# Kernel optimization log

Hardware: AMD Instinct MI355X
Metric: run time of the kernel (lower is better)

The kernel has to match this reference:

```python
import jax, jax.numpy as jnp
import numpy as np

HIDDEN = 2048
NUM_HEADS = 16
HEAD_DIM = HIDDEN // NUM_HEADS
SCALE = 1.0 / np.sqrt(HEAD_DIM).astype(np.float32)
BATCH, SEQ = 2, 2048


def setup_inputs() -> dict:
    key = jax.random.key(0)
    ks = jax.random.split(key, 9)
    std = 0.02
    inp = {
        'hidden_states': jax.random.normal(ks[0], (BATCH, SEQ, HIDDEN), jnp.float32),
        'attention_mask': jnp.zeros((BATCH, 1, 1, SEQ), jnp.float32),
        'Wq': jax.random.normal(ks[1], (HIDDEN, HIDDEN), jnp.float32) * std,
        'bq': jnp.zeros((HIDDEN,), jnp.float32),
        'Wk': jax.random.normal(ks[2], (HIDDEN, HIDDEN), jnp.float32) * std,
        'bk': jnp.zeros((HIDDEN,), jnp.float32),
        'Wv': jax.random.normal(ks[3], (HIDDEN, HIDDEN), jnp.float32) * std,
        'bv': jnp.zeros((HIDDEN,), jnp.float32),
        'Wo': jax.random.normal(ks[4], (HIDDEN, HIDDEN), jnp.float32) * std,
        'bo': jnp.zeros((HIDDEN,), jnp.float32),
    }
    return inp


def _split_heads(x):
    b, s, _ = x.shape
    return x.reshape(b, s, NUM_HEADS, HEAD_DIM).transpose(0, 2, 1, 3)  # [b,h,s,d]


def reference(hidden_states, attention_mask, Wq, bq, Wk, bk, Wv, bv, Wo, bo):
    # Linear layers (torch convention: y = x @ W.T + b)
    q = _split_heads(hidden_states @ Wq.T + bq)
    k = _split_heads(hidden_states @ Wk.T + bk)
    v = _split_heads(hidden_states @ Wv.T + bv)
    scores = jnp.einsum('bhqd,bhkd->bhqk', q, k) * SCALE
    scores = scores + attention_mask
    weights = jax.nn.softmax(scores, axis=-1)  # dropout is identity in eval
    ctx = jnp.einsum('bhqk,bhkd->bhqd', weights, v)
    b, h, s, d = ctx.shape
    ctx = ctx.transpose(0, 2, 1, 3).reshape(b, s, HIDDEN)
    return ctx @ Wo.T + bo
```

## Files before the change

kernel.cpp:

```cpp
#include <hip/hip_runtime.h>

typedef __bf16 bf16_t;
typedef bf16_t bf16x8 __attribute__((ext_vector_type(8)));
typedef float f32x4 __attribute__((ext_vector_type(4)));

#define HIDDEN 2048
#define SEQ 2048
#define BATCH 2
#define NHEADS 16
#define HDIM 128
#define MTOT (BATCH*SEQ)
#define SCALE 0.088388347648318447f
#define C1EXP2 0.12753102158508967f
#define LOG2E  1.4426950408889634f

__device__ __forceinline__ float dev_exp2(float x) { return __builtin_amdgcn_exp2f(x); }

typedef __attribute__((address_space(1))) const void gvoid_t;
typedef __attribute__((address_space(3))) void svoid_t;
__device__ __forceinline__ void async_copy16(const bf16_t* g, bf16_t* l) {
  __builtin_amdgcn_global_load_lds((gvoid_t*)g, (svoid_t*)l, 16, 0, 0);
}

__global__ void cvt_all(const float* __restrict__ x,  const float* __restrict__ wq,
                        const float* __restrict__ wk, const float* __restrict__ wv,
                        const float* __restrict__ wo,
                        bf16_t* __restrict__ xb, bf16_t* __restrict__ wqkb,
                        bf16_t* __restrict__ wvb, bf16_t* __restrict__ wob) {
  const size_t HH = (size_t)HIDDEN * HIDDEN;
  const float* src; bf16_t* dst;
  switch (blockIdx.y) {
    case 0:  src = x;        dst = xb;        break;
    case 1:  src = x + HH;   dst = xb + HH;   break;
    case 2:  src = wq;       dst = wqkb;      break;
    case 3:  src = wk;       dst = wqkb + HH; break;
    case 4:  src = wv;       dst = wvb;       break;
    default: src = wo;       dst = wob;       break;
  }
  int i = blockIdx.x * 256 + threadIdx.x;
  float4 v = reinterpret_cast<const float4*>(src)[i];
  union { bf16_t h[4]; uint2 u; } t;
  t.h[0] = (bf16_t)v.x; t.h[1] = (bf16_t)v.y; t.h[2] = (bf16_t)v.z; t.h[3] = (bf16_t)v.w;
  reinterpret_cast<uint2*>(dst)[i] = t.u;
}

__global__ void pack_bias2(const float* __restrict__ a, const float* __restrict__ b2,
                           float* __restrict__ out) {
  int i = blockIdx.x * 256 + threadIdx.x;
  out[i] = (i < HIDDEN) ? a[i] : b2[i - HIDDEN];
}

template<bool OUT_BF16, bool ROW_BIAS>
__global__ __launch_bounds__(256, 2)
void gemm_bt(const bf16_t* __restrict__ A, const bf16_t* __restrict__ Bt,
             const float* __restrict__ bias, void* __restrict__ Yv,
             int M, int N, int K, int ldY) {
  __shared__ __align__(16) bf16_t As[128 * 32];
  __shared__ __align__(16) bf16_t Bs[128 * 32];
  const int tid  = threadIdx.x;
  const int lane = tid & 63;
  const int wv   = tid >> 6;
  const int wr   = wv >> 1, wc = wv & 1;
  const int lr   = lane & 15, quad = lane >> 4;
  const int n0   = blockIdx.x * 128;
  const int m0   = blockIdx.y * 128;

  f32x4 acc[4][4] = {};

  const int srow = wv * 16 + (lane >> 2);
  const int scol = (lane & 3) * 8;
  const bf16_t* gA = A  + (size_t)(m0 + srow) * K + scol;
  const bf16_t* gB = Bt + (size_t)(n0 + srow) * K + scol;
  bf16_t* lA = &As[wv * 16 * 32];
  bf16_t* lB = &Bs[wv * 16 * 32];
  const size_t step64 = (size_t)64 * K;

  for (int kt = 0; kt < K; kt += 32) {
    __syncthreads();
    async_copy16(gA,          lA);
    async_copy16(gA + step64, lA + 64 * 32);
    async_copy16(gB,          lB);
    async_copy16(gB + step64, lB + 64 * 32);
    gA += 32; gB += 32;
    __syncthreads();
    bf16x8 af[4], bfr[4];
#pragma unroll
    for (int mi = 0; mi < 4; ++mi)
      af[mi] = *(const bf16x8*)&As[(wr * 64 + mi * 16 + lr) * 32 + quad * 8];
#pragma unroll
    for (int ni = 0; ni < 4; ++ni)
      bfr[ni] = *(const bf16x8*)&Bs[(wc * 64 + ni * 16 + lr) * 32 + quad * 8];
#pragma unroll
    for (int mi = 0; mi < 4; ++mi)
#pragma unroll
      for (int ni = 0; ni < 4; ++ni)
        acc[mi][ni] = __builtin_amdgcn_mfma_f32_16x16x32_bf16(af[mi], bfr[ni], acc[mi][ni], 0, 0, 0);
  }

  float bcol[4];
  if (!ROW_BIAS) {
#pragma unroll
    for (int ni = 0; ni < 4; ++ni) bcol[ni] = bias[n0 + wc * 64 + ni * 16 + lr];
  }
#pragma unroll
  for (int mi = 0; mi < 4; ++mi) {
#pragma unroll
    for (int r = 0; r < 4; ++r) {
      int row = m0 + wr * 64 + mi * 16 + quad * 4 + r;
      float brow = ROW_BIAS ? bias[row] : 0.0f;
      size_t base = (size_t)row * ldY + n0 + wc * 64;
#pragma unroll
      for (int ni = 0; ni < 4; ++ni) {
        float y = acc[mi][ni][r] + (ROW_BIAS ? brow : bcol[ni]);
        int col = ni * 16 + lr;
        if (OUT_BF16) ((bf16_t*)Yv)[base + col] = (bf16_t)y;
        else          ((float*)Yv)[base + col]  = y;
      }
    }
  }
}

#define BQ 128
#define BKV 64
#define LDQK 4096

__global__ __launch_bounds__(256, 2)
void attn_kernel(const bf16_t* __restrict__ QK, const bf16_t* __restrict__ Vt,
                 const float* __restrict__ mask, bf16_t* __restrict__ O) {
  __shared__ __align__(16) bf16_t Ks[2][BKV * 128];
  __shared__ __align__(16) bf16_t Vs[2][HDIM * BKV];
  __shared__ __align__(16) bf16_t Ps[BQ * BKV];

  const int tid  = threadIdx.x;
  const int lane = tid & 63;
  const int wv   = tid >> 6;
  const int lr   = lane & 15, quad = lane >> 4;
  const int q0   = blockIdx.x * BQ;
  const int bh   = blockIdx.y;
  const int b    = bh >> 4, h = bh & 15;

  const bf16_t* Qg = QK + (size_t)(b * SEQ + q0) * LDQK + h * HDIM;
  const bf16_t* Kg = QK + (size_t)(b * SEQ) * LDQK + HIDDEN + h * HDIM;
  const bf16_t* Vg = Vt + (size_t)(h * HDIM) * MTOT + b * SEQ;
  const float*  mb = mask + b * SEQ;

  bf16x8 qf[2][4];
#pragma unroll
  for (int mi = 0; mi < 2; ++mi)
#pragma unroll
    for (int dk = 0; dk < 4; ++dk)
      qf[mi][dk] = *(const bf16x8*)(Qg + (size_t)(wv * 32 + mi * 16 + lr) * LDQK + dk * 32 + quad * 8);

  const int kcs = lane & 15;
  const int vcs = lane & 7;
  const bf16_t* kgp[4]; const bf16_t* vgp[4];
  int lKo[4], lVo[4];
#pragma unroll
  for (int i = 0; i < 4; ++i) {
    int kr = i * 16 + wv * 4 + (lane >> 4);
    kgp[i] = Kg + (size_t)kr * LDQK + ((kcs ^ (kr & 15)) * 8);
    lKo[i] = (i * 16 + wv * 4) * 128;
    int vr = i * 32 + wv * 8 + (lane >> 3);
    vgp[i] = Vg + (size_t)vr * MTOT + ((vcs ^ (vr & 7)) * 8);
    lVo[i] = (i * 32 + wv * 8) * 64;
  }

  float l_st[2][4] = {};
  f32x4 oacc[2][8] = {};

#pragma unroll
  for (int i = 0; i < 4; ++i) async_copy16(kgp[i], &Ks[0][lKo[i]]);
#pragma unroll
  for (int i = 0; i < 4; ++i) async_copy16(vgp[i], &Vs[0][lVo[i]]);

  for (int kt = 0; kt < SEQ; kt += 2 * BKV) {
#pragma unroll
    for (int half = 0; half < 2; ++half) {
      const int cur  = half;
      const int kcur = kt + half * BKV;
      __syncthreads();
      const int knext = kcur + BKV;
      if (knext < SEQ) {
#pragma unroll
        for (int i = 0; i < 4; ++i) async_copy16(kgp[i] + (size_t)knext * LDQK, &Ks[cur ^ 1][lKo[i]]);
#pragma unroll
        for (int i = 0; i < 4; ++i) async_copy16(vgp[i] + knext, &Vs[cur ^ 1][lVo[i]]);
      }

      float mk[4];
#pragma unroll
      for (int ni = 0; ni < 4; ++ni) mk[ni] = mb[kcur + ni * 16 + lr] * LOG2E;

      f32x4 sacc[2][4] = {};
#pragma unroll
      for (int dk = 0; dk < 4; ++dk) {
        bf16x8 kf[4];
#pragma unroll
        for (int ni = 0; ni < 4; ++ni)
          kf[ni] = *(const bf16x8*)&Ks[cur][(ni * 16 + lr) * 128 + (((dk * 4 + quad) ^ lr) * 8)];
#pragma unroll
        for (int mi = 0; mi < 2; ++mi)
#pragma unroll
          for (int ni = 0; ni < 4; ++ni)
            sacc[mi][ni] = __builtin_amdgcn_mfma_f32_16x16x32_bf16(qf[mi][dk], kf[ni], sacc[mi][ni], 0, 0, 0);
      }

#pragma unroll
      for (int mi = 0; mi < 2; ++mi) {
#pragma unroll
        for (int r = 0; r < 4; ++r) {
          float p0 = dev_exp2(fmaf(sacc[mi][0][r], C1EXP2, mk[0]));
          float p1 = dev_exp2(fmaf(sacc[mi][1][r], C1EXP2, mk[1]));
          float p2 = dev_exp2(fmaf(sacc[mi][2][r], C1EXP2, mk[2]));
          float p3 = dev_exp2(fmaf(sacc[mi][3][r], C1EXP2, mk[3]));
          int pr = wv * 32 + mi * 16 + quad * 4 + r;
          int key = pr & 7;
          Ps[pr * BKV + (((0 + (lr >> 3)) ^ key) * 8) + (lr & 7)] = (bf16_t)p0;
          Ps[pr * BKV + (((2 + (lr >> 3)) ^ key) * 8) + (lr & 7)] = (bf16_t)p1;
          Ps[pr * BKV + (((4 + (lr >> 3)) ^ key) * 8) + (lr & 7)] = (bf16_t)p2;
          Ps[pr * BKV + (((6 + (lr >> 3)) ^ key) * 8) + (lr & 7)] = (bf16_t)p3;
          l_st[mi][r] += (p0 + p1) + (p2 + p3);
        }
      }

#pragma unroll
      for (int ki = 0; ki < 2; ++ki) {
        bf16x8 pf[2];
#pragma unroll
        for (int mi = 0; mi < 2; ++mi)
          pf[mi] = *(const bf16x8*)&Ps[(wv * 32 + mi * 16 + lr) * BKV + (((ki * 4 + quad) ^ (lr & 7)) * 8)];
#pragma unroll
        for (int di = 0; di < 8; ++di) {
          bf16x8 vf = *(const bf16x8*)&Vs[cur][(di * 16 + lr) * BKV + (((ki * 4 + quad) ^ (lr & 7)) * 8)];
#pragma unroll
          for (int mi = 0; mi < 2; ++mi)
            oacc[mi][di] = __builtin_amdgcn_mfma_f32_16x16x32_bf16(pf[mi], vf, oacc[mi][di], 0, 0, 0);
        }
      }
    }
  }

  bf16_t* Ob = O + (size_t)(b * SEQ + q0) * HIDDEN + h * HDIM;
#pragma unroll
  for (int mi = 0; mi < 2; ++mi) {
#pragma unroll
    for (int r = 0; r < 4; ++r) {
      float s = l_st[mi][r];
      s += __shfl_xor(s, 1);
      s += __shfl_xor(s, 2);
      s += __shfl_xor(s, 4);
      s += __shfl_xor(s, 8);
      float inv = 1.0f / s;
      size_t rowoff = (size_t)(wv * 32 + mi * 16 + quad * 4 + r) * HIDDEN;
#pragma unroll
      for (int di = 0; di < 8; ++di)
        Ob[rowoff + di * 16 + lr] = (bf16_t)(oacc[mi][di][r] * inv);
    }
  }
}

extern "C" void kernel_launch(void* const* d_in, const int* in_sizes, int n_in,
                              void* d_out, int out_size, void* d_ws, size_t ws_size,
                              hipStream_t stream) {
  const float* x   = (const float*)d_in[0];
  const float* msk = (const float*)d_in[1];
  const float* Wq  = (const float*)d_in[2];
  const float* bq  = (const float*)d_in[3];
  const float* Wk  = (const float*)d_in[4];
  const float* bk  = (const float*)d_in[5];
  const float* Wv  = (const float*)d_in[6];
  const float* bv  = (const float*)d_in[7];
  const float* Wo  = (const float*)d_in[8];
  const float* bo  = (const float*)d_in[9];
  float* out = (float*)d_out;

  bf16_t* Xb   = (bf16_t*)d_ws;
  bf16_t* Wqkb = Xb   + (size_t)MTOT * HIDDEN;
  bf16_t* Wvb  = Wqkb + (size_t)2 * HIDDEN * HIDDEN;
  bf16_t* Wob  = Wvb  + (size_t)HIDDEN * HIDDEN;
  bf16_t* QKo  = Wob  + (size_t)HIDDEN * HIDDEN;
  bf16_t* Vto  = QKo  + (size_t)MTOT * 2 * HIDDEN;
  float*  bqk  = (float*)(Vto + (size_t)HIDDEN * MTOT);
  bf16_t* Cb   = Xb;

  cvt_all<<<dim3(HIDDEN * HIDDEN / 4 / 256, 6), 256, 0, stream>>>(
      x, Wq, Wk, Wv, Wo, Xb, Wqkb, Wvb, Wob);
  pack_bias2<<<2 * HIDDEN / 256, 256, 0, stream>>>(bq, bk, bqk);

  gemm_bt<true, false><<<dim3(32, 32), 256, 0, stream>>>(Xb, Wqkb, bqk, QKo,
                                                         MTOT, 2 * HIDDEN, HIDDEN, 2 * HIDDEN);
  gemm_bt<true, true><<<dim3(32, 16), 256, 0, stream>>>(Wvb, Xb, bv, Vto,
                                                        HIDDEN, MTOT, HIDDEN, MTOT);
  attn_kernel<<<dim3(SEQ / BQ, BATCH * NHEADS), 256, 0, stream>>>(QKo, Vto, msk, Cb);
  gemm_bt<false, false><<<dim3(16, 32), 256, 0, stream>>>(Cb, Wob, bo, out,
                                                          MTOT, HIDDEN, HIDDEN, HIDDEN);
}
```

Baseline: 419.2 us.

## Shrink attention tile to 64 queries with 2 waves, drop K/V double buffering

The attention kernel now uses 64-query blocks with 128 threads and loads each K/V tile into a single LDS buffer, synchronising before and after each load instead of prefetching the next tile. This halves LDS use per block and doubles the grid, so more blocks can be resident per CU. In exchange, load latency is no longer overlapped with compute, and each K/V tile is fetched by twice as many blocks. The GEMM launch bound is also raised from 2 to 3 blocks per CU, which pressures the compiler to use fewer registers.

```diff
diff --git a/kernel.cpp b/kernel.cpp
--- a/kernel.cpp
+++ b/kernel.cpp
@@ -51,7 +51,7 @@
 }
 
 template<bool OUT_BF16, bool ROW_BIAS>
-__global__ __launch_bounds__(256, 2)
+__global__ __launch_bounds__(256, 3)
 void gemm_bt(const bf16_t* __restrict__ A, const bf16_t* __restrict__ Bt,
              const float* __restrict__ bias, void* __restrict__ Yv,
              int M, int N, int K, int ldY) {
@@ -120,15 +120,15 @@
   }
 }
 
-#define BQ 128
+#define BQ 64
 #define BKV 64
 #define LDQK 4096
 
-__global__ __launch_bounds__(256, 2)
+__global__ __launch_bounds__(128, 2)
 void attn_kernel(const bf16_t* __restrict__ QK, const bf16_t* __restrict__ Vt,
                  const float* __restrict__ mask, bf16_t* __restrict__ O) {
-  __shared__ __align__(16) bf16_t Ks[2][BKV * 128];
-  __shared__ __align__(16) bf16_t Vs[2][HDIM * BKV];
+  __shared__ __align__(16) bf16_t Ks[BKV * 128];
+  __shared__ __align__(16) bf16_t Vs[HDIM * BKV];
   __shared__ __align__(16) bf16_t Ps[BQ * BKV];
 
   const int tid  = threadIdx.x;
@@ -153,89 +153,77 @@
 
   const int kcs = lane & 15;
   const int vcs = lane & 7;
-  const bf16_t* kgp[4]; const bf16_t* vgp[4];
-  int lKo[4], lVo[4];
-#pragma unroll
-  for (int i = 0; i < 4; ++i) {
-    int kr = i * 16 + wv * 4 + (lane >> 4);
+  const bf16_t* kgp[8]; const bf16_t* vgp[8];
+  int lKo[8], lVo[8];
+#pragma unroll
+  for (int i = 0; i < 8; ++i) {
+    int kr = wv * 32 + i * 4 + (lane >> 4);
     kgp[i] = Kg + (size_t)kr * LDQK + ((kcs ^ (kr & 15)) * 8);
-    lKo[i] = (i * 16 + wv * 4) * 128;
-    int vr = i * 32 + wv * 8 + (lane >> 3);
+    lKo[i] = (wv * 32 + i * 4) * 128;
+    int vr = wv * 64 + i * 8 + (lane >> 3);
     vgp[i] = Vg + (size_t)vr * MTOT + ((vcs ^ (vr & 7)) * 8);
-    lVo[i] = (i * 32 + wv * 8) * 64;
+    lVo[i] = (wv * 64 + i * 8) * 64;
   }
 
   float l_st[2][4] = {};
   f32x4 oacc[2][8] = {};
 
-#pragma unroll
-  for (int i = 0; i < 4; ++i) async_copy16(kgp[i], &Ks[0][lKo[i]]);
-#pragma unroll
-  for (int i = 0; i < 4; ++i) async_copy16(vgp[i], &Vs[0][lVo[i]]);
-
-  for (int kt = 0; kt < SEQ; kt += 2 * BKV) {
-#pragma unroll
-    for (int half = 0; half < 2; ++half) {
-      const int cur  = half;
-      const int kcur = kt + half * BKV;
-      __syncthreads();
-      const int knext = kcur + BKV;
-      if (knext < SEQ) {
-#pragma unroll
-        for (int i = 0; i < 4; ++i) async_copy16(kgp[i] + (size_t)knext * LDQK, &Ks[cur ^ 1][lKo[i]]);
-#pragma unroll
-        for (int i = 0; i < 4; ++i) async_copy16(vgp[i] + knext, &Vs[cur ^ 1][lVo[i]]);
+  for (int kt = 0; kt < SEQ; kt += BKV) {
+    __syncthreads();
+#pragma unroll
+    for (int i = 0; i < 8; ++i) async_copy16(kgp[i] + (size_t)kt * LDQK, &Ks[lKo[i]]);
+#pragma unroll
+    for (int i = 0; i < 8; ++i) async_copy16(vgp[i] + kt, &Vs[lVo[i]]);
+    __syncthreads();
+
+    float mk[4];
+#pragma unroll
+    for (int ni = 0; ni < 4; ++ni) mk[ni] = mb[kt + ni * 16 + lr] * LOG2E;
+
+    f32x4 sacc[2][4] = {};
+#pragma unroll
+    for (int dk = 0; dk < 4; ++dk) {
+      bf16x8 kf[4];
+#pragma unroll
+      for (int ni = 0; ni < 4; ++ni)
+        kf[ni] = *(const bf16x8*)&Ks[(ni * 16 + lr) * 128 + (((dk * 4 + quad) ^ lr) * 8)];
+#pragma unroll
+      for (int mi = 0; mi < 2; ++mi)
+#pragma unroll
+        for (int ni = 0; ni < 4; ++ni)
+          sacc[mi][ni] = __builtin_amdgcn_mfma_f32_16x16x32_bf16(qf[mi][dk], kf[ni], sacc[mi][ni], 0, 0, 0);
+    }
+
+#pragma unroll
+    for (int mi = 0; mi < 2; ++mi) {
+#pragma unroll
+      for (int r = 0; r < 4; ++r) {
+        float p0 = dev_exp2(fmaf(sacc[mi][0][r], C1EXP2, mk[0]));
+        float p1 = dev_exp2(fmaf(sacc[mi][1][r], C1EXP2, mk[1]));
+        float p2 = dev_exp2(fmaf(sacc[mi][2][r], C1EXP2, mk[2]));
+        float p3 = dev_exp2(fmaf(sacc[mi][3][r], C1EXP2, mk[3]));
+        int pr = wv * 32 + mi * 16 + quad * 4 + r;
+        int key = pr & 7;
+        Ps[pr * BKV + (((0 + (lr >> 3)) ^ key) * 8) + (lr & 7)] = (bf16_t)p0;
+        Ps[pr * BKV + (((2 + (lr >> 3)) ^ key) * 8) + (lr & 7)] = (bf16_t)p1;
+        Ps[pr * BKV + (((4 + (lr >> 3)) ^ key) * 8) + (lr & 7)] = (bf16_t)p2;
+        Ps[pr * BKV + (((6 + (lr >> 3)) ^ key) * 8) + (lr & 7)] = (bf16_t)p3;
+        l_st[mi][r] += (p0 + p1) + (p2 + p3);
       }
-
-      float mk[4];
-#pragma unroll
-      for (int ni = 0; ni < 4; ++ni) mk[ni] = mb[kcur + ni * 16 + lr] * LOG2E;
-
-      f32x4 sacc[2][4] = {};
-#pragma unroll
-      for (int dk = 0; dk < 4; ++dk) {
-        bf16x8 kf[4];
-#pragma unroll
-        for (int ni = 0; ni < 4; ++ni)
-          kf[ni] = *(const bf16x8*)&Ks[cur][(ni * 16 + lr) * 128 + (((dk * 4 + quad) ^ lr) * 8)];
+    }
+
+#pragma unroll
+    for (int ki = 0; ki < 2; ++ki) {
+      bf16x8 pf[2];
+#pragma unroll
+      for (int mi = 0; mi < 2; ++mi)
+        pf[mi] = *(const bf16x8*)&Ps[(wv * 32 + mi * 16 + lr) * BKV + (((ki * 4 + quad) ^ (lr & 7)) * 8)];
+#pragma unroll
+      for (int di = 0; di < 8; ++di) {
+        bf16x8 vf = *(const bf16x8*)&Vs[(di * 16 + lr) * BKV + (((ki * 4 + quad) ^ (lr & 7)) * 8)];
 #pragma unroll
         for (int mi = 0; mi < 2; ++mi)
-#pragma unroll
-          for (int ni = 0; ni < 4; ++ni)
-            sacc[mi][ni] = __builtin_amdgcn_mfma_f32_16x16x32_bf16(qf[mi][dk], kf[ni], sacc[mi][ni], 0, 0, 0);
-      }
-
-#pragma unroll
-      for (int mi = 0; mi < 2; ++mi) {
-#pragma unroll
-        for (int r = 0; r < 4; ++r) {
-          float p0 = dev_exp2(fmaf(sacc[mi][0][r], C1EXP2, mk[0]));
-          float p1 = dev_exp2(fmaf(sacc[mi][1][r], C1EXP2, mk[1]));
-          float p2 = dev_exp2(fmaf(sacc[mi][2][r], C1EXP2, mk[2]));
-          float p3 = dev_exp2(fmaf(sacc[mi][3][r], C1EXP2, mk[3]));
-          int pr = wv * 32 + mi * 16 + quad * 4 + r;
-          int key = pr & 7;
-          Ps[pr * BKV + (((0 + (lr >> 3)) ^ key) * 8) + (lr & 7)] = (bf16_t)p0;
-          Ps[pr * BKV + (((2 + (lr >> 3)) ^ key) * 8) + (lr & 7)] = (bf16_t)p1;
-          Ps[pr * BKV + (((4 + (lr >> 3)) ^ key) * 8) + (lr & 7)] = (bf16_t)p2;
-          Ps[pr * BKV + (((6 + (lr >> 3)) ^ key) * 8) + (lr & 7)] = (bf16_t)p3;
-          l_st[mi][r] += (p0 + p1) + (p2 + p3);
-        }
-      }
-
-#pragma unroll
-      for (int ki = 0; ki < 2; ++ki) {
-        bf16x8 pf[2];
-#pragma unroll
-        for (int mi = 0; mi < 2; ++mi)
-          pf[mi] = *(const bf16x8*)&Ps[(wv * 32 + mi * 16 + lr) * BKV + (((ki * 4 + quad) ^ (lr & 7)) * 8)];
-#pragma unroll
-        for (int di = 0; di < 8; ++di) {
-          bf16x8 vf = *(const bf16x8*)&Vs[cur][(di * 16 + lr) * BKV + (((ki * 4 + quad) ^ (lr & 7)) * 8)];
-#pragma unroll
-          for (int mi = 0; mi < 2; ++mi)
-            oacc[mi][di] = __builtin_amdgcn_mfma_f32_16x16x32_bf16(pf[mi], vf, oacc[mi][di], 0, 0, 0);
-        }
+          oacc[mi][di] = __builtin_amdgcn_mfma_f32_16x16x32_bf16(pf[mi], vf, oacc[mi][di], 0, 0, 0);
       }
     }
   }
@@ -291,7 +279,7 @@
                                                          MTOT, 2 * HIDDEN, HIDDEN, 2 * HIDDEN);
   gemm_bt<true, true><<<dim3(32, 16), 256, 0, stream>>>(Wvb, Xb, bv, Vto,
                                                         HIDDEN, MTOT, HIDDEN, MTOT);
-  attn_kernel<<<dim3(SEQ / BQ, BATCH * NHEADS), 256, 0, stream>>>(QKo, Vto, msk, Cb);
+  attn_kernel<<<dim3(SEQ / BQ, BATCH * NHEADS), 128, 0, stream>>>(QKo, Vto, msk, Cb);
   gemm_bt<false, false><<<dim3(16, 32), 256, 0, stream>>>(Cb, Wob, bo, out,
                                                           MTOT, HIDDEN, HIDDEN, HIDDEN);
 }
```

Result: no change. 415.0 us (-1.0%).
